# Optimization experiments

Measured on AMD Instinct MI355X. Metric: run time of the kernel, lower is better.

Reference implementation:

```python
import jax, jax.numpy as jnp
import numpy as np

GAMMA = 0.00390625  # 1/256


def setup_inputs() -> dict:
    key = jax.random.key(0)
    ks = jax.random.split(key, 8)
    B, F, S = 65536, 256, 1024
    return {
        "x": jax.random.normal(ks[0], (B, F), dtype=jnp.float32),
        "sv": jax.random.normal(ks[1], (S, F), dtype=jnp.float32),
        "W1": jax.random.normal(ks[2], (S, S), dtype=jnp.float32) * (1.0 / np.sqrt(S)),
        "b1": jax.random.normal(ks[3], (S,), dtype=jnp.float32) * 0.01,
        "W2": jax.random.normal(ks[4], (S, S), dtype=jnp.float32) * (1.0 / np.sqrt(S)),
        "b2": jax.random.normal(ks[5], (S,), dtype=jnp.float32) * 0.01,
        "Wh": jax.random.normal(ks[6], (2, S), dtype=jnp.float32) * (1.0 / np.sqrt(S)),
        "bh": jax.random.normal(ks[7], (2,), dtype=jnp.float32) * 0.01,
    }


def reference(x, sv, W1, b1, W2, b2, Wh, bh):
    # RBF kernel features: k[b, s] = exp(-gamma * ||x_b - sv_s||^2)
    # Expand squared distance to avoid a (B, S, F) intermediate.
    x2 = jnp.sum(x * x, axis=-1, keepdims=True)          # (B, 1)
    s2 = jnp.sum(sv * sv, axis=-1)[None, :]              # (1, S)
    d2 = x2 + s2 - 2.0 * jnp.einsum("bf,sf->bs", x, sv)  # (B, S)
    k = jnp.exp(-GAMMA * d2)                              # (B, S)
    # MLP classifier: depth=2 hidden ReLU layers + 2-logit head
    h = jax.nn.relu(jnp.einsum("bs,os->bo", k, W1) + b1)
    h = jax.nn.relu(jnp.einsum("bs,os->bo", h, W2) + b2)
    return jnp.einsum("bs,os->bo", h, Wh) + bh           # (B, 2)
```

## Files before the change

kernel.cpp:

```cpp
#include <hip/hip_runtime.h>

typedef _Float16 f16x8 __attribute__((ext_vector_type(8)));
typedef _Float16 f16x4 __attribute__((ext_vector_type(4)));
typedef float    f32x4 __attribute__((ext_vector_type(4)));

#define GAMMA_F 0.00390625f

__global__ __launch_bounds__(256) void prep_rows_kernel(
    const float* __restrict__ src, _Float16* __restrict__ dst,
    float* __restrict__ sq, int nrows)
{
    int lane = threadIdx.x & 63, w = threadIdx.x >> 6;
    int row = blockIdx.x * 4 + w;
    if (row >= nrows) return;
    float4 v = ((const float4*)(src + (size_t)row * 256))[lane];
    f16x4 h;
    h[0] = (_Float16)v.x; h[1] = (_Float16)v.y;
    h[2] = (_Float16)v.z; h[3] = (_Float16)v.w;
    *((f16x4*)(dst + (size_t)row * 256) + lane) = h;
    float ss = v.x*v.x + v.y*v.y + v.z*v.z + v.w*v.w;
#pragma unroll
    for (int off = 32; off; off >>= 1) ss += __shfl_down(ss, off);
    if (lane == 0) sq[row] = ss;
}

__global__ __launch_bounds__(256) void cvt_kernel(
    const float* __restrict__ src, _Float16* __restrict__ dst, int n4)
{
    int i = blockIdx.x * 256 + threadIdx.x;
    if (i < n4) {
        float4 v = ((const float4*)src)[i];
        f16x4 h;
        h[0] = (_Float16)v.x; h[1] = (_Float16)v.y;
        h[2] = (_Float16)v.z; h[3] = (_Float16)v.w;
        ((f16x4*)dst)[i] = h;
    }
}

#define SBAR()   __builtin_amdgcn_s_barrier()
#define RFENCE() asm volatile("" ::: "memory")

#define GLDA(gptr, uoff)                                                       \
    asm volatile("s_mov_b32 m0, %1\n\t"                                        \
                 "global_load_lds_dwordx4 %0, off\n\t"                         \
                 "s_mov_b32 m0, -1"                                            \
                 :: "v"((const void*)(gptr)), "s"(uoff))

#define UOF(x) __builtin_amdgcn_readfirstlane((x) + wb)

#define STA(s, h) do {                                                         \
    GLDA(aP##h##0, UOF((s)*32768 + (h)*16384));                                \
    GLDA(aP##h##1, UOF((s)*32768 + (h)*16384 + 8192));                         \
} while (0)
#define STB(s, h) do {                                                         \
    GLDA(bP##h##0, UOF(65536 + (s)*32768 + (h)*16384));                        \
    GLDA(bP##h##1, UOF(65536 + (s)*32768 + (h)*16384 + 8192));                 \
} while (0)
#define ADV_A() do { aP00+=64; aP01+=64; aP10+=64; aP11+=64; } while (0)
#define ADV_B() do { bP00+=64; bP01+=64; bP10+=64; bP11+=64; } while (0)

#define PRE_A(s, mh) do { _Pragma("unroll") for (int mi = 0; mi < 4; ++mi)     \
    a0f[mi] = *(const f16x8*)(ldsb + aO0 + (s)*32768 + (mh)*8192 + mi*2048);   \
} while (0)
#define POST_A(s, mh) do { _Pragma("unroll") for (int mi = 0; mi < 4; ++mi)    \
    a1f[mi] = *(const f16x8*)(ldsb + aO1 + (s)*32768 + (mh)*8192 + mi*2048);   \
} while (0)
#define PRE_BA(s, nh) do { _Pragma("unroll") for (int nb = 0; nb < 2; ++nb)    \
    bA0[nb] = *(const f16x8*)(ldsb + bO0 + (s)*32768 + (nh)*4096 + nb*2048);   \
} while (0)
#define POST_BA(s, nh) do { _Pragma("unroll") for (int nb = 0; nb < 2; ++nb)   \
    bA1[nb] = *(const f16x8*)(ldsb + bO1 + (s)*32768 + (nh)*4096 + nb*2048);   \
} while (0)
#define PRE_BB(s, nh) do { _Pragma("unroll") for (int nb = 0; nb < 2; ++nb)    \
    bB0[nb] = *(const f16x8*)(ldsb + bO0 + (s)*32768 + (nh)*4096 + nb*2048);   \
} while (0)
#define POST_BB(s, nh) do { _Pragma("unroll") for (int nb = 0; nb < 2; ++nb)   \
    bB1[nb] = *(const f16x8*)(ldsb + bO1 + (s)*32768 + (nh)*4096 + nb*2048);   \
} while (0)

#define MFMA8(af, bf, mh, nh) do {                                             \
    _Pragma("unroll") for (int mi = 0; mi < 4; ++mi)                           \
    _Pragma("unroll") for (int nb = 0; nb < 2; ++nb)                           \
        acc[(mh)*4+mi][(nh)*2+nb] = __builtin_amdgcn_mfma_f32_16x16x32_f16(    \
            af[mi], bf[nb], acc[(mh)*4+mi][(nh)*2+nb], 0, 0, 0);               \
} while (0)

template <int MODE, int K>
__global__ __launch_bounds__(512, 1) void gemm256_kernel(
    const _Float16* __restrict__ A, const _Float16* __restrict__ B,
    _Float16* __restrict__ C, const float* __restrict__ e0,
    const float* __restrict__ e1)
{
    constexpr int KT = K / 64;
    constexpr int NITER = KT / 2;
    __shared__ f16x8 lds[8192];
    char* ldsb = (char*)lds;

    const int t    = threadIdx.x;
    const int lane = t & 63, w = t >> 6;
    const int wb   = w << 10;
    const int wr   = w >> 2, wc = w & 3;
    const int lrow = lane & 15, kq = lane >> 4;

    int poison = 0;
    asm volatile("" : "+v"(poison));
    if (poison) lds[0] = f16x8{};

    int bid  = blockIdx.x;
    int cpx  = (int)(gridDim.x >> 3);
    int lbid = (bid & 7) * cpx + (bid >> 3);
    int bm   = lbid >> 2, bn = lbid & 3;
    int rowA0 = bm * 256, rowB0 = bn * 256;

    const int aO0 = ((wr*128 + lrow)*8 + ( kq      ^ (lrow & 7))) * 16;
    const int aO1 = ((wr*128 + lrow)*8 + ((4 + kq) ^ (lrow & 7))) * 16;
    const int bO0 = 65536 + ((wc*64 + lrow)*8 + ( kq      ^ (lrow & 7))) * 16;
    const int bO1 = 65536 + ((wc*64 + lrow)*8 + ((4 + kq) ^ (lrow & 7))) * 16;

    const int prow = t >> 3;
    const int cg   = (t & 7) ^ (prow & 7);
    const _Float16* aP00 = A + (size_t)(rowA0 + prow      ) * K + cg * 8;
    const _Float16* aP01 = aP00 + (size_t) 64 * K;
    const _Float16* aP10 = aP00 + (size_t)128 * K;
    const _Float16* aP11 = aP00 + (size_t)192 * K;
    const _Float16* bP00 = B + (size_t)(rowB0 + prow      ) * K + cg * 8;
    const _Float16* bP01 = bP00 + (size_t) 64 * K;
    const _Float16* bP10 = bP00 + (size_t)128 * K;
    const _Float16* bP11 = bP00 + (size_t)192 * K;

    f32x4 acc[8][4];
#pragma unroll
    for (int i = 0; i < 8; ++i)
#pragma unroll
        for (int j = 0; j < 4; ++j) acc[i][j] = (f32x4){0.f, 0.f, 0.f, 0.f};

    f16x8 a0f[4], a1f[4], bA0[2], bA1[2], bB0[2], bB1[2];

    STA(0,0); STA(0,1); STB(0,0); STB(0,1); ADV_A(); ADV_B();
    STA(1,0); STA(1,1); STB(1,0); STB(1,1); ADV_A(); ADV_B();
    asm volatile("s_waitcnt vmcnt(8)" ::: "memory");
    SBAR();

    for (int j = 0; j < NITER; ++j) {
        const bool last = (j == NITER - 1);

        RFENCE();
        PRE_A(0, 0); PRE_BA(0, 0);
        if (j > 0) STA(1, 0);
        SBAR();
        POST_A(0, 0); POST_BA(0, 0);
        __builtin_amdgcn_s_setprio(1);
        MFMA8(a0f, bA0, 0, 0); MFMA8(a1f, bA1, 0, 0);
        __builtin_amdgcn_s_setprio(0);
        RFENCE();
        PRE_BB(0, 1);
        if (j > 0) { STA(1, 1); ADV_A(); }
        SBAR();
        POST_BB(0, 1);
        __builtin_amdgcn_s_setprio(1);
        MFMA8(a0f, bB0, 0, 1); MFMA8(a1f, bB1, 0, 1);
        __builtin_amdgcn_s_setprio(0);
        RFENCE();
        PRE_A(0, 1);
        if (!last) STB(0, 0);
        SBAR();
        POST_A(0, 1);
        __builtin_amdgcn_s_setprio(1);
        MFMA8(a0f, bA0, 1, 0); MFMA8(a1f, bA1, 1, 0);
        __builtin_amdgcn_s_setprio(0);
        RFENCE();
        if (!last) {
            STB(0, 1); ADV_B();
            asm volatile("s_waitcnt vmcnt(4)" ::: "memory");
        } else {
            asm volatile("s_waitcnt vmcnt(0)" ::: "memory");
        }
        SBAR();
        __builtin_amdgcn_s_setprio(1);
        MFMA8(a0f, bB0, 1, 1); MFMA8(a1f, bB1, 1, 1);
        __builtin_amdgcn_s_setprio(0);
        RFENCE();
        PRE_A(1, 0); PRE_BA(1, 0);
        if (!last) STA(0, 0);
        SBAR();
        POST_A(1, 0); POST_BA(1, 0);
        __builtin_amdgcn_s_setprio(1);
        MFMA8(a0f, bA0, 0, 0); MFMA8(a1f, bA1, 0, 0);
        __builtin_amdgcn_s_setprio(0);
        RFENCE();
        PRE_BB(1, 1);
        if (!last) { STA(0, 1); ADV_A(); }
        SBAR();
        POST_BB(1, 1);
        __builtin_amdgcn_s_setprio(1);
        MFMA8(a0f, bB0, 0, 1); MFMA8(a1f, bB1, 0, 1);
        __builtin_amdgcn_s_setprio(0);
        RFENCE();
        PRE_A(1, 1);
        if (!last) STB(1, 0);
        SBAR();
        POST_A(1, 1);
        __builtin_amdgcn_s_setprio(1);
        MFMA8(a0f, bA0, 1, 0); MFMA8(a1f, bA1, 1, 0);
        __builtin_amdgcn_s_setprio(0);
        RFENCE();
        if (!last) {
            STB(1, 1); ADV_B();
            asm volatile("s_waitcnt vmcnt(4)" ::: "memory");
        }
        SBAR();
        __builtin_amdgcn_s_setprio(1);
        MFMA8(a0f, bB0, 1, 1); MFMA8(a1f, bB1, 1, 1);
        __builtin_amdgcn_s_setprio(0);
    }

    int gr0 = rowA0 + wr * 128;
    int gc0 = rowB0 + wc * 64;
    float ecol[4];
#pragma unroll
    for (int ni = 0; ni < 4; ++ni)
        ecol[ni] = (MODE == 0) ? e1[gc0 + ni * 16 + lrow]
                               : e0[gc0 + ni * 16 + lrow];
#pragma unroll
    for (int mi = 0; mi < 8; ++mi) {
#pragma unroll
        for (int jj = 0; jj < 4; ++jj) {
            int row = gr0 + mi * 16 + kq * 4 + jj;
            float xr = (MODE == 0) ? e0[row] : 0.f;
            size_t base = (size_t)row * 1024 + gc0 + lrow;
#pragma unroll
            for (int ni = 0; ni < 4; ++ni) {
                float v = acc[mi][ni][jj];
                if (MODE == 0) {
                    v = __expf(-GAMMA_F * (xr + ecol[ni] - 2.f * v));
                } else {
                    v += ecol[ni];
                    v = fmaxf(v, 0.f);
                }
                C[base + (size_t)ni * 16] = (_Float16)v;
            }
        }
    }
}

__global__ __launch_bounds__(256) void head_kernel(
    const _Float16* __restrict__ h2, const float* __restrict__ Wh,
    const float* __restrict__ bh, float* __restrict__ out)
{
    int lane = threadIdx.x & 63, w = threadIdx.x >> 6;
    int row = blockIdx.x * 4 + w;
    const _Float16* hp = h2 + (size_t)row * 1024;
    float s0 = 0.f, s1 = 0.f;
#pragma unroll
    for (int i = 0; i < 2; ++i) {
        int base = (i * 64 + lane) * 8;
        f16x8 hv = *(const f16x8*)(hp + base);
#pragma unroll
        for (int j = 0; j < 8; ++j) {
            float hj = (float)hv[j];
            s0 = fmaf(hj, Wh[base + j], s0);
            s1 = fmaf(hj, Wh[1024 + base + j], s1);
        }
    }
#pragma unroll
    for (int off = 32; off; off >>= 1) {
        s0 += __shfl_down(s0, off);
        s1 += __shfl_down(s1, off);
    }
    if (lane == 0) {
        out[(size_t)row * 2 + 0] = s0 + bh[0];
        out[(size_t)row * 2 + 1] = s1 + bh[1];
    }
}

extern "C" void kernel_launch(void* const* d_in, const int* in_sizes, int n_in,
                              void* d_out, int out_size, void* d_ws, size_t ws_size,
                              hipStream_t stream)
{
    const float* x  = (const float*)d_in[0];
    const float* sv = (const float*)d_in[1];
    const float* W1 = (const float*)d_in[2];
    const float* b1 = (const float*)d_in[3];
    const float* W2 = (const float*)d_in[4];
    const float* b2 = (const float*)d_in[5];
    const float* Wh = (const float*)d_in[6];
    const float* bh = (const float*)d_in[7];
    float* out = (float*)d_out;
    char* ws = (char*)d_ws;

    constexpr size_t OFF_SV = 0;
    constexpr size_t OFF_W1 = OFF_SV + 524288;
    constexpr size_t OFF_W2 = OFF_W1 + 2097152;
    constexpr size_t OFF_S2 = OFF_W2 + 2097152;
    constexpr size_t PERSIST = OFF_S2 + 4096;

    _Float16* svf = (_Float16*)(ws + OFF_SV);
    _Float16* w1f = (_Float16*)(ws + OFF_W1);
    _Float16* w2f = (_Float16*)(ws + OFF_W2);
    float*    s2v = (float*)(ws + OFF_S2);

    int Bc = 65536;
    while (Bc > 256 && PERSIST + (size_t)Bc * 4100ULL > ws_size) Bc >>= 1;

    char* chunk_base = ws + PERSIST;
    _Float16* kb  = (_Float16*)chunk_base;
    _Float16* h1b = (_Float16*)(chunk_base + (size_t)Bc * 2048);
    _Float16* xf  = h1b;
    float*    x2v = (float*)(chunk_base + (size_t)Bc * 4096);

    prep_rows_kernel<<<1024 / 4, 256, 0, stream>>>(sv, svf, s2v, 1024);
    cvt_kernel<<<1024, 256, 0, stream>>>(W1, w1f, 262144);
    cvt_kernel<<<1024, 256, 0, stream>>>(W2, w2f, 262144);

    int nchunks = 65536 / Bc;
    int ggrid   = (Bc / 256) * 4;
    for (int c = 0; c < nchunks; ++c) {
        const float* xc = x + (size_t)c * Bc * 256;
        prep_rows_kernel<<<Bc / 4, 256, 0, stream>>>(xc, xf, x2v, Bc);
        gemm256_kernel<0, 256><<<ggrid, 512, 0, stream>>>(xf, svf, kb, x2v, s2v);
        gemm256_kernel<1, 1024><<<ggrid, 512, 0, stream>>>(kb, w1f, h1b, b1, nullptr);
        gemm256_kernel<1, 1024><<<ggrid, 512, 0, stream>>>(h1b, w2f, kb, b2, nullptr);
        head_kernel<<<Bc / 4, 256, 0, stream>>>(kb, Wh, bh, out + (size_t)c * Bc * 2);
    }
}
```

Baseline: 380.9 us.

## Merge GEMM phases into four per k-tile pair to halve barriers

The main GEMM loop is restructured from eight barrier-separated phases of 16 MFMAs into four phases of 32 MFMAs. Each phase loads both B halves up front and issues global-to-LDS loads in larger groups. This halves the s_barrier and fence count per iteration, cutting synchronization overhead. In exchange it holds more fragment registers live at once and gives coarser interleaving of LDS reads with MFMA work.

After: 372.7 us. -2.2%, faster.

```diff
diff --git a/kernel.cpp b/kernel.cpp
--- a/kernel.cpp
+++ b/kernel.cpp
@@ -59,22 +59,22 @@
 #define ADV_A() do { aP00+=64; aP01+=64; aP10+=64; aP11+=64; } while (0)
 #define ADV_B() do { bP00+=64; bP01+=64; bP10+=64; bP11+=64; } while (0)
 
-#define PRE_A(s, mh) do { _Pragma("unroll") for (int mi = 0; mi < 4; ++mi)     \
+#define RD_A0(s, mh) do { _Pragma("unroll") for (int mi = 0; mi < 4; ++mi)     \
     a0f[mi] = *(const f16x8*)(ldsb + aO0 + (s)*32768 + (mh)*8192 + mi*2048);   \
 } while (0)
-#define POST_A(s, mh) do { _Pragma("unroll") for (int mi = 0; mi < 4; ++mi)    \
+#define RD_A1(s, mh) do { _Pragma("unroll") for (int mi = 0; mi < 4; ++mi)     \
     a1f[mi] = *(const f16x8*)(ldsb + aO1 + (s)*32768 + (mh)*8192 + mi*2048);   \
 } while (0)
-#define PRE_BA(s, nh) do { _Pragma("unroll") for (int nb = 0; nb < 2; ++nb)    \
+#define RD_B0A(s, nh) do { _Pragma("unroll") for (int nb = 0; nb < 2; ++nb)    \
     bA0[nb] = *(const f16x8*)(ldsb + bO0 + (s)*32768 + (nh)*4096 + nb*2048);   \
 } while (0)
-#define POST_BA(s, nh) do { _Pragma("unroll") for (int nb = 0; nb < 2; ++nb)   \
+#define RD_B1A(s, nh) do { _Pragma("unroll") for (int nb = 0; nb < 2; ++nb)    \
     bA1[nb] = *(const f16x8*)(ldsb + bO1 + (s)*32768 + (nh)*4096 + nb*2048);   \
 } while (0)
-#define PRE_BB(s, nh) do { _Pragma("unroll") for (int nb = 0; nb < 2; ++nb)    \
+#define RD_B0B(s, nh) do { _Pragma("unroll") for (int nb = 0; nb < 2; ++nb)    \
     bB0[nb] = *(const f16x8*)(ldsb + bO0 + (s)*32768 + (nh)*4096 + nb*2048);   \
 } while (0)
-#define POST_BB(s, nh) do { _Pragma("unroll") for (int nb = 0; nb < 2; ++nb)   \
+#define RD_B1B(s, nh) do { _Pragma("unroll") for (int nb = 0; nb < 2; ++nb)    \
     bB1[nb] = *(const f16x8*)(ldsb + bO1 + (s)*32768 + (nh)*4096 + nb*2048);   \
 } while (0)
 
@@ -83,6 +83,13 @@
     _Pragma("unroll") for (int nb = 0; nb < 2; ++nb)                           \
         acc[(mh)*4+mi][(nh)*2+nb] = __builtin_amdgcn_mfma_f32_16x16x32_f16(    \
             af[mi], bf[nb], acc[(mh)*4+mi][(nh)*2+nb], 0, 0, 0);               \
+} while (0)
+
+#define MFMA32(mh) do {                                                        \
+    __builtin_amdgcn_s_setprio(1);                                             \
+    MFMA8(a0f, bA0, mh, 0); MFMA8(a1f, bA1, mh, 0);                            \
+    MFMA8(a0f, bB0, mh, 1); MFMA8(a1f, bB1, mh, 1);                            \
+    __builtin_amdgcn_s_setprio(0);                                             \
 } while (0)
 
 template <int MODE, int K>
@@ -145,73 +152,37 @@
         const bool last = (j == NITER - 1);
 
         RFENCE();
-        PRE_A(0, 0); PRE_BA(0, 0);
-        if (j > 0) STA(1, 0);
-        SBAR();
-        POST_A(0, 0); POST_BA(0, 0);
-        __builtin_amdgcn_s_setprio(1);
-        MFMA8(a0f, bA0, 0, 0); MFMA8(a1f, bA1, 0, 0);
-        __builtin_amdgcn_s_setprio(0);
-        RFENCE();
-        PRE_BB(0, 1);
-        if (j > 0) { STA(1, 1); ADV_A(); }
-        SBAR();
-        POST_BB(0, 1);
-        __builtin_amdgcn_s_setprio(1);
-        MFMA8(a0f, bB0, 0, 1); MFMA8(a1f, bB1, 0, 1);
-        __builtin_amdgcn_s_setprio(0);
-        RFENCE();
-        PRE_A(0, 1);
-        if (!last) STB(0, 0);
-        SBAR();
-        POST_A(0, 1);
-        __builtin_amdgcn_s_setprio(1);
-        MFMA8(a0f, bA0, 1, 0); MFMA8(a1f, bA1, 1, 0);
-        __builtin_amdgcn_s_setprio(0);
-        RFENCE();
+        RD_A0(0, 0); RD_B0A(0, 0); RD_B0B(0, 1);
+        if (j > 0) { STA(1, 0); STA(1, 1); ADV_A(); }
+        SBAR();
+        RD_A1(0, 0); RD_B1A(0, 0); RD_B1B(0, 1);
+        MFMA32(0);
+        RFENCE();
+        RD_A0(0, 1);
         if (!last) {
-            STB(0, 1); ADV_B();
+            STB(0, 0); STB(0, 1); ADV_B();
             asm volatile("s_waitcnt vmcnt(4)" ::: "memory");
         } else {
             asm volatile("s_waitcnt vmcnt(0)" ::: "memory");
         }
         SBAR();
-        __builtin_amdgcn_s_setprio(1);
-        MFMA8(a0f, bB0, 1, 1); MFMA8(a1f, bB1, 1, 1);
-        __builtin_amdgcn_s_setprio(0);
-        RFENCE();
-        PRE_A(1, 0); PRE_BA(1, 0);
-        if (!last) STA(0, 0);
-        SBAR();
-        POST_A(1, 0); POST_BA(1, 0);
-        __builtin_amdgcn_s_setprio(1);
-        MFMA8(a0f, bA0, 0, 0); MFMA8(a1f, bA1, 0, 0);
-        __builtin_amdgcn_s_setprio(0);
-        RFENCE();
-        PRE_BB(1, 1);
-        if (!last) { STA(0, 1); ADV_A(); }
-        SBAR();
-        POST_BB(1, 1);
-        __builtin_amdgcn_s_setprio(1);
-        MFMA8(a0f, bB0, 0, 1); MFMA8(a1f, bB1, 0, 1);
-        __builtin_amdgcn_s_setprio(0);
-        RFENCE();
-        PRE_A(1, 1);
-        if (!last) STB(1, 0);
-        SBAR();
-        POST_A(1, 1);
-        __builtin_amdgcn_s_setprio(1);
-        MFMA8(a0f, bA0, 1, 0); MFMA8(a1f, bA1, 1, 0);
-        __builtin_amdgcn_s_setprio(0);
-        RFENCE();
+        RD_A1(0, 1);
+        MFMA32(1);
+        RFENCE();
+        RD_A0(1, 0); RD_B0A(1, 0); RD_B0B(1, 1);
+        if (!last) { STA(0, 0); STA(0, 1); ADV_A(); }
+        SBAR();
+        RD_A1(1, 0); RD_B1A(1, 0); RD_B1B(1, 1);
+        MFMA32(0);
+        RFENCE();
+        RD_A0(1, 1);
         if (!last) {
-            STB(1, 1); ADV_B();
+            STB(1, 0); STB(1, 1); ADV_B();
             asm volatile("s_waitcnt vmcnt(4)" ::: "memory");
         }
         SBAR();
-        __builtin_amdgcn_s_setprio(1);
-        MFMA8(a0f, bB0, 1, 1); MFMA8(a1f, bB1, 1, 1);
-        __builtin_amdgcn_s_setprio(0);
+        RD_A1(1, 1);
+        MFMA32(1);
     }
 
     int gr0 = rowA0 + wr * 128;
```
